# Optimization experiments

Measured on AMD Instinct MI355X. Metric: run time of the kernel, lower is better.

## Reference

```python
import jax, jax.numpy as jnp
import numpy as np

EMBED_DIM = 768
NUM_HEADS = 12
HEAD_DIM = EMBED_DIM // NUM_HEADS
B, T = 2, 2048


def setup_inputs() -> dict:
    key = jax.random.key(0)
    kx, kq, kqb, ko, kob = jax.random.split(key, 5)
    x = jax.random.normal(kx, (B, T, EMBED_DIM), dtype=jnp.float32)
    # xavier-uniform style params
    lim_qkv = float(np.sqrt(6.0 / (EMBED_DIM + 3 * EMBED_DIM)))
    qkv_kernel = jax.random.uniform(kq, (EMBED_DIM, 3 * EMBED_DIM), minval=-lim_qkv, maxval=lim_qkv, dtype=jnp.float32)
    qkv_bias = jnp.zeros((3 * EMBED_DIM,), dtype=jnp.float32)
    lim_o = float(np.sqrt(6.0 / (EMBED_DIM + EMBED_DIM)))
    o_kernel = jax.random.uniform(ko, (EMBED_DIM, EMBED_DIM), minval=-lim_o, maxval=lim_o, dtype=jnp.float32)
    o_bias = jnp.zeros((EMBED_DIM,), dtype=jnp.float32)
    return {"x": x, "qkv_kernel": qkv_kernel, "qkv_bias": qkv_bias, "o_kernel": o_kernel, "o_bias": o_bias}


def reference(x, qkv_kernel, qkv_bias, o_kernel, o_bias):
    b, t, d = x.shape
    # fused QKV projection
    qkv = jnp.einsum('btd,de->bte', x, qkv_kernel) + qkv_bias  # [B,T,3D]
    qkv = qkv.reshape(b, t, 3, NUM_HEADS, HEAD_DIM).transpose(2, 0, 3, 1, 4)  # [3,B,H,T,Dh]
    q, k, v = qkv[0], qkv[1], qkv[2]
    # naive attention: materializes full [B,H,T,T] scores (as in original)
    scale = 1.0 / np.sqrt(HEAD_DIM).astype(np.float32)
    attn_logits = jnp.einsum('bhqd,bhkd->bhqk', q, k) * scale
    attention = jax.nn.softmax(attn_logits, axis=-1)
    values = jnp.einsum('bhqk,bhkd->bhqd', attention, v)
    values = values.transpose(0, 2, 1, 3).reshape(b, t, d)  # [B,T,D]
    o = jnp.einsum('btd,de->bte', values, o_kernel) + o_bias
    return (o, attention)
```

## Files before the change

### kernel.cpp

```cpp
#include <hip/hip_runtime.h>
#include <hip/hip_bf16.h>
#include <hip/hip_fp16.h>

typedef _Float16 f16;
typedef _Float16 f16x4 __attribute__((ext_vector_type(4)));
typedef _Float16 f16x8 __attribute__((ext_vector_type(8)));
typedef float f32x4 __attribute__((ext_vector_type(4)));

#define MFMA16(a, b, c) __builtin_amdgcn_mfma_f32_16x16x32_f16(a, b, c, 0, 0, 0)

__device__ __forceinline__ float fexp2(float x) {
#if __has_builtin(__builtin_amdgcn_exp2f)
    return __builtin_amdgcn_exp2f(x);
#else
    return exp2f(x);
#endif
}

typedef __attribute__((address_space(1))) const void gconst_t;
typedef __attribute__((address_space(3))) void lds_t;
__device__ __forceinline__ void gload16(const f16* g, f16* l) {
    __builtin_amdgcn_global_load_lds((gconst_t*)g, (lds_t*)l, 16, 0, 0);
}

__global__ void k_convert_x(const float* __restrict__ in, f16* __restrict__ out, int n4) {
    int i = blockIdx.x * blockDim.x + threadIdx.x;
    if (i >= n4) return;
    float4 v = ((const float4*)in)[i];
    f16x4 o = {(f16)v.x, (f16)v.y, (f16)v.z, (f16)v.w};
    ((f16x4*)out)[i] = o;
}

__global__ __launch_bounds__(256) void k_transpose(const float* __restrict__ in,
                                                   f16* __restrict__ out, int K, int N) {
    __shared__ f16 tile[64][72];
    int n0 = blockIdx.x * 64, k0 = blockIdx.y * 64;
    int t = threadIdx.x;
    int r = t >> 2, cb = (t & 3) * 16;
    const float* src = in + (size_t)(k0 + r) * N + n0 + cb;
#pragma unroll
    for (int j = 0; j < 4; ++j) {
        float4 v = ((const float4*)src)[j];
        tile[r][cb + 4 * j + 0] = (f16)v.x;
        tile[r][cb + 4 * j + 1] = (f16)v.y;
        tile[r][cb + 4 * j + 2] = (f16)v.z;
        tile[r][cb + 4 * j + 3] = (f16)v.w;
    }
    __syncthreads();
    int nl = t >> 2, kb = (t & 3) * 16;
    f16* dst = out + (size_t)(n0 + nl) * K + k0 + kb;
#pragma unroll
    for (int j = 0; j < 2; ++j) {
        f16x8 o;
#pragma unroll
        for (int e = 0; e < 8; ++e) o[e] = tile[kb + 8 * j + e][nl];
        *(f16x8*)(dst + 8 * j) = o;
    }
}

__device__ __forceinline__ void gemm_core(const f16* __restrict__ A, const f16* __restrict__ Bt,
                                          int m0, int n0, int lane, int w, int wr, int wc,
                                          f16* As, f16* Bs, f32x4 acc[4][4]) {
    int prow = lane >> 2, pc = lane & 3;
    int lrow = prow ^ ((prow >> 2) & 1);
    int lcol = (pc ^ (lrow & 3)) * 8;
    int rsw = (lane & 7) << 3;
    for (int kt = 0; kt < 24; ++kt) {
        const f16* ab = A + (size_t)(m0 + w * 32 + lrow) * 768 + kt * 32 + lcol;
        const f16* bb = Bt + (size_t)(n0 + w * 32 + lrow) * 768 + kt * 32 + lcol;
        gload16(ab, As + (w * 32) * 32);
        gload16(ab + (size_t)16 * 768, As + (w * 32 + 16) * 32);
        gload16(bb, Bs + (w * 32) * 32);
        gload16(bb + (size_t)16 * 768, Bs + (w * 32 + 16) * 32);
        __syncthreads();
        f16x8 a[4], b[4];
#pragma unroll
        for (int i = 0; i < 4; ++i) {
            int idx = (wr * 64 + i * 16 + (lane & 15)) * 32 + (lane >> 4) * 8;
            a[i] = *(const f16x8*)(As + (idx ^ rsw));
        }
#pragma unroll
        for (int j = 0; j < 4; ++j) {
            int idx = (wc * 64 + j * 16 + (lane & 15)) * 32 + (lane >> 4) * 8;
            b[j] = *(const f16x8*)(Bs + (idx ^ rsw));
        }
#pragma unroll
        for (int i = 0; i < 4; ++i)
#pragma unroll
            for (int j = 0; j < 4; ++j) acc[i][j] = MFMA16(a[i], b[j], acc[i][j]);
        __syncthreads();
    }
}

__global__ __launch_bounds__(256) void k_qkv_gemm(const f16* __restrict__ A, const f16* __restrict__ Bt,
                                                  const float* __restrict__ bias,
                                                  f16* __restrict__ Qh, f16* __restrict__ Kf,
                                                  f16* __restrict__ Vf) {
    __shared__ __align__(16) f16 As[128 * 32];
    __shared__ __align__(16) f16 Bs[128 * 32];
    int m0 = blockIdx.x * 128, n0 = blockIdx.y * 128;
    int t = threadIdx.x, lane = t & 63, w = t >> 6;
    int wr = w >> 1, wc = w & 1;
    f32x4 zero = {0.f, 0.f, 0.f, 0.f};
    f32x4 acc[4][4];
#pragma unroll
    for (int i = 0; i < 4; ++i)
#pragma unroll
        for (int j = 0; j < 4; ++j) acc[i][j] = zero;

    gemm_core(A, Bt, m0, n0, lane, w, wr, wc, As, Bs, acc);

    const float QSCALE = 0.18033688011112042f;
#pragma unroll
    for (int j = 0; j < 4; ++j) {
        int n = n0 + wc * 64 + j * 16 + (lane & 15);
        int which = n / 768;
        int rem = n - which * 768;
        int h = rem >> 6, d = rem & 63;
        float bv = bias[n];
#pragma unroll
        for (int i = 0; i < 4; ++i) {
            int m = m0 + wr * 64 + i * 16 + ((lane >> 4) << 2);
            int bb = m >> 11, tt = m & 2047;
            int bh = bb * 12 + h;
            if (which == 2) {
                int kt = tt >> 6;
                int half = (tt & 63) >> 5, hi = (tt & 31) >> 3, e0 = tt & 7;
                int jd = d >> 4, lo = d & 15;
                size_t addr = (((size_t)bh * 32 + kt) * 8 + jd * 2 + half) * 512 +
                              (size_t)(hi * 16 + lo) * 8 + e0;
                f16x4 pk;
#pragma unroll
                for (int r = 0; r < 4; ++r) pk[r] = (f16)(acc[i][j][r] + bv);
                *(f16x4*)(Vf + addr) = pk;
            } else if (which == 0) {
#pragma unroll
                for (int r = 0; r < 4; ++r)
                    Qh[((size_t)bh * 2048 + tt + r) * 64 + d] = (f16)((acc[i][j][r] + bv) * QSCALE);
            } else {
                int half = d >> 5, hi = (d & 31) >> 3, e = d & 7;
#pragma unroll
                for (int r = 0; r < 4; ++r) {
                    int tr = tt + r;
                    int kt = tr >> 6, row = tr & 63;
                    int s = row >> 4, lo = row & 15;
                    size_t addr = (((size_t)bh * 32 + kt) * 8 + s * 2 + half) * 512 +
                                  (size_t)(hi * 16 + lo) * 8 + e;
                    Kf[addr] = (f16)(acc[i][j][r] + bv);
                }
            }
        }
    }
}

__global__ __launch_bounds__(256) void k_o_gemm(const f16* __restrict__ A, const f16* __restrict__ Bt,
                                                const float* __restrict__ bias,
                                                float* __restrict__ out) {
    __shared__ __align__(16) f16 As[128 * 32];
    __shared__ __align__(16) f16 Bs[128 * 32];
    int m0 = blockIdx.x * 128, n0 = blockIdx.y * 128;
    int t = threadIdx.x, lane = t & 63, w = t >> 6;
    int wr = w >> 1, wc = w & 1;
    f32x4 zero = {0.f, 0.f, 0.f, 0.f};
    f32x4 acc[4][4];
#pragma unroll
    for (int i = 0; i < 4; ++i)
#pragma unroll
        for (int j = 0; j < 4; ++j) acc[i][j] = zero;

    gemm_core(A, Bt, m0, n0, lane, w, wr, wc, As, Bs, acc);

#pragma unroll
    for (int j = 0; j < 4; ++j) {
        int n = n0 + wc * 64 + j * 16 + (lane & 15);
        float bv = bias[n];
#pragma unroll
        for (int i = 0; i < 4; ++i) {
            int m = m0 + wr * 64 + i * 16 + ((lane >> 4) << 2);
#pragma unroll
            for (int r = 0; r < 4; ++r) out[(size_t)(m + r) * 768 + n] = acc[i][j][r] + bv;
        }
    }
}

__global__ __launch_bounds__(256) void k_lsum(const f16* __restrict__ Qh, const f16* __restrict__ Kf,
                                              float* __restrict__ lpart) {
    int qt = blockIdx.x, bh = blockIdx.y, kc = blockIdx.z;
    int q0 = qt * 64;
    int t = threadIdx.x, lane = t & 63, w = t >> 6;
    const f16* qbase = Qh + ((size_t)bh * 2048 + q0 + w * 16) * 64;
    const f16* kfb = Kf + (size_t)bh * 32 * 4096 + (size_t)lane * 8;

    f16x8 aq[2];
#pragma unroll
    for (int f = 0; f < 2; ++f)
        aq[f] = *(const f16x8*)(qbase + (size_t)(lane & 15) * 64 + f * 32 + (lane >> 4) * 8);
    f32x4 zero = {0.f, 0.f, 0.f, 0.f};

    auto LOADK = [&](f16x8* dst, int kt) {
        const f16* kp = kfb + (size_t)kt * 4096;
#pragma unroll
        for (int f = 0; f < 8; ++f) dst[f] = *(const f16x8*)(kp + f * 512);
    };
    auto QKTS = [&](const f16x8* kf, f32x4* s4) {
#pragma unroll
        for (int s = 0; s < 4; ++s) {
            s4[s] = MFMA16(kf[2 * s], aq[0], zero);
            s4[s] = MFMA16(kf[2 * s + 1], aq[1], s4[s]);
        }
    };

    f16x8 ka[8], kb2[8];
    float lsum = 0.f;
    int base = kc * 8;
    LOADK(ka, base);
    for (int i = 0; i < 8; i += 2) {
        f32x4 s4[4];
        LOADK(kb2, base + i + 1);
        QKTS(ka, s4);
#pragma unroll
        for (int s = 0; s < 4; ++s)
#pragma unroll
            for (int r = 0; r < 4; ++r) lsum += fexp2(s4[s][r]);
        LOADK(ka, base + ((i + 2) & 7));
        QKTS(kb2, s4);
#pragma unroll
        for (int s = 0; s < 4; ++s)
#pragma unroll
            for (int r = 0; r < 4; ++r) lsum += fexp2(s4[s][r]);
    }
    lsum += __shfl_xor(lsum, 16, 64);
    lsum += __shfl_xor(lsum, 32, 64);
    float* lp = lpart + (size_t)kc * 49152 + (size_t)bh * 2048 + q0 + w * 16;
    if (lane < 16) lp[lane] = lsum;
}

__global__ __launch_bounds__(256, 3) void k_attn(const f16* __restrict__ Qh, const f16* __restrict__ Kf,
                                                 const f16* __restrict__ Vf,
                                                 const float* __restrict__ lpart,
                                                 float* __restrict__ attn, f16* __restrict__ valh) {
    __shared__ __align__(16) float Ps32_all[4][16 * 68];
    int orig = blockIdx.x;
    int swz = (orig & 7) * 96 + (orig >> 3);
    int bh = swz >> 5, qt = swz & 31;
    int q0 = qt * 64;
    int t = threadIdx.x, lane = t & 63, w = t >> 6;

    const f16* qbase = Qh + ((size_t)bh * 2048 + q0 + w * 16) * 64;
    const f16* kfb = Kf + (size_t)bh * 32 * 4096 + (size_t)lane * 8;
    const f16* vfb = Vf + (size_t)bh * 32 * 4096 + (size_t)lane * 8;

    f16x8 aq[2];
#pragma unroll
    for (int f = 0; f < 2; ++f)
        aq[f] = *(const f16x8*)(qbase + (size_t)(lane & 15) * 64 + f * 32 + (lane >> 4) * 8);
    f32x4 zero = {0.f, 0.f, 0.f, 0.f};

    float linv;
    {
        size_t qoff = (size_t)bh * 2048 + q0 + w * 16 + (lane & 15);
        float s = 0.f;
#pragma unroll
        for (int kc = 0; kc < 4; ++kc) s += lpart[(size_t)kc * 49152 + qoff];
        linv = 1.0f / s;
    }

    auto LOADK = [&](f16x8* dst, int kt) {
        const f16* kp = kfb + (size_t)kt * 4096;
#pragma unroll
        for (int f = 0; f < 8; ++f) dst[f] = *(const f16x8*)(kp + f * 512);
    };
    auto QKTS = [&](const f16x8* kf, f32x4* s4) {
#pragma unroll
        for (int s = 0; s < 4; ++s) {
            s4[s] = MFMA16(kf[2 * s], aq[0], zero);
            s4[s] = MFMA16(kf[2 * s + 1], aq[1], s4[s]);
        }
    };

    f32x4 accv[4];
#pragma unroll
    for (int j = 0; j < 4; ++j) accv[j] = zero;
    float* Ps = Ps32_all[w];
    float* attn_base = attn + ((size_t)bh * 2048 + q0 + w * 16) * 2048;
    f16x8 ka[8], kb2[8], vbuf[8];

    auto step2 = [&](f16x8* curK, f16x8* nxtK, int kt) {
        {
            const f16* vp = vfb + (size_t)kt * 4096;
#pragma unroll
            for (int f = 0; f < 8; ++f) vbuf[f] = *(const f16x8*)(vp + f * 512);
        }
        LOADK(nxtK, (kt + 1) & 31);
        f32x4 s4[4];
        QKTS(curK, s4);
#pragma unroll
        for (int s = 0; s < 4; ++s) {
            f32x4 pv;
#pragma unroll
            for (int r = 0; r < 4; ++r) pv[r] = fexp2(s4[s][r]) * linv;
            *(f32x4*)(Ps + (lane & 15) * 68 + s * 16 + (lane >> 4) * 4) = pv;
        }
        f16x8 pa[2];
#pragma unroll
        for (int half = 0; half < 2; ++half) {
            const float* pr = Ps + (lane & 15) * 68 + half * 32 + (lane >> 4) * 8;
            f32x4 lo = *(const f32x4*)(pr);
            f32x4 hi = *(const f32x4*)(pr + 4);
            f16x8 pf = {(f16)lo[0], (f16)lo[1], (f16)lo[2], (f16)lo[3],
                        (f16)hi[0], (f16)hi[1], (f16)hi[2], (f16)hi[3]};
            pa[half] = pf;
        }
        float* ab = attn_base + kt * 64;
#pragma unroll
        for (int i = 0; i < 4; ++i) {
            int row = i * 4 + (lane >> 4);
            int col = (lane & 15) * 4;
            f32x4 v = *(const f32x4*)(Ps + row * 68 + col);
            *(f32x4*)(ab + (size_t)row * 2048 + col) = v;
        }
#pragma unroll
        for (int jd = 0; jd < 4; ++jd) {
            accv[jd] = MFMA16(pa[0], vbuf[2 * jd], accv[jd]);
            accv[jd] = MFMA16(pa[1], vbuf[2 * jd + 1], accv[jd]);
        }
    };

    LOADK(ka, 0);
    for (int kt = 0; kt < 32; kt += 2) {
        step2(ka, kb2, kt);
        step2(kb2, ka, kt + 1);
    }

    int b = bh / 12, h = bh - b * 12;
#pragma unroll
    for (int j = 0; j < 4; ++j) {
#pragma unroll
        for (int r = 0; r < 4; ++r) {
            int rowg = b * 2048 + q0 + w * 16 + (lane >> 4) * 4 + r;
            int col = h * 64 + j * 16 + (lane & 15);
            valh[(size_t)rowg * 768 + col] = (f16)accv[j][r];
        }
    }
}

extern "C" void kernel_launch(void* const* d_in, const int* in_sizes, int n_in,
                              void* d_out, int out_size, void* d_ws, size_t ws_size,
                              hipStream_t stream) {
    const float* x = (const float*)d_in[0];
    const float* wqkv = (const float*)d_in[1];
    const float* bqkv = (const float*)d_in[2];
    const float* wo = (const float*)d_in[3];
    const float* bo = (const float*)d_in[4];

    float* out_o = (float*)d_out;
    float* out_attn = out_o + (size_t)2 * 2048 * 768;

    f16* ws = (f16*)d_ws;
    f16* xh = ws;
    f16* wqkv_t = xh + 3145728;
    f16* wo_t = wqkv_t + 1769472;
    f16* Qh = wo_t + 589824;
    f16* Kf = Qh + 3145728;
    f16* Vf = Kf + 3145728;
    f16* valh = Vf + 3145728;
    float* lpart = (float*)(valh + 3145728);

    k_convert_x<<<3072, 256, 0, stream>>>(x, xh, 786432);
    k_transpose<<<dim3(36, 12), 256, 0, stream>>>(wqkv, wqkv_t, 768, 2304);
    k_transpose<<<dim3(12, 12), 256, 0, stream>>>(wo, wo_t, 768, 768);
    k_qkv_gemm<<<dim3(32, 18), 256, 0, stream>>>(xh, wqkv_t, bqkv, Qh, Kf, Vf);
    k_lsum<<<dim3(32, 24, 4), 256, 0, stream>>>(Qh, Kf, lpart);
    k_attn<<<768, 256, 0, stream>>>(Qh, Kf, Vf, lpart, out_attn, valh);
    k_o_gemm<<<dim3(32, 6), 256, 0, stream>>>(valh, wo_t, bo, out_o);
}
```

Measured before the change: 203.2 us.

## Stage K/V tiles through LDS in attention, merge prep kernels, add MFMA priority

The attention kernel now loads each K/V tile once per block into double-buffered LDS with global_load_lds, instead of every wave loading the full tiles into registers. This is meant to cut redundant global traffic and register pressure, at the cost of a block-wide barrier every iteration and more LDS per block, which may lower occupancy. The three preprocessing launches (x conversion and two weight transposes) are merged into one kernel to save launch overhead. s_setprio hints are placed around the MFMA sections in the lsum and attention kernels.

```diff
diff --git a/kernel.cpp b/kernel.cpp
--- a/kernel.cpp
+++ b/kernel.cpp
@@ -23,19 +23,9 @@
     __builtin_amdgcn_global_load_lds((gconst_t*)g, (lds_t*)l, 16, 0, 0);
 }
 
-__global__ void k_convert_x(const float* __restrict__ in, f16* __restrict__ out, int n4) {
-    int i = blockIdx.x * blockDim.x + threadIdx.x;
-    if (i >= n4) return;
-    float4 v = ((const float4*)in)[i];
-    f16x4 o = {(f16)v.x, (f16)v.y, (f16)v.z, (f16)v.w};
-    ((f16x4*)out)[i] = o;
-}
-
-__global__ __launch_bounds__(256) void k_transpose(const float* __restrict__ in,
-                                                   f16* __restrict__ out, int K, int N) {
-    __shared__ f16 tile[64][72];
-    int n0 = blockIdx.x * 64, k0 = blockIdx.y * 64;
-    int t = threadIdx.x;
+__device__ __forceinline__ void transpose_body(const float* __restrict__ in, f16* __restrict__ out,
+                                               int K, int N, int n0, int k0, int t,
+                                               f16 (*tile)[72]) {
     int r = t >> 2, cb = (t & 3) * 16;
     const float* src = in + (size_t)(k0 + r) * N + n0 + cb;
 #pragma unroll
@@ -55,6 +45,27 @@
 #pragma unroll
         for (int e = 0; e < 8; ++e) o[e] = tile[kb + 8 * j + e][nl];
         *(f16x8*)(dst + 8 * j) = o;
+    }
+}
+
+__global__ __launch_bounds__(256) void k_prep(const float* __restrict__ x,
+                                              const float* __restrict__ wqkv,
+                                              const float* __restrict__ wo,
+                                              f16* __restrict__ xh, f16* __restrict__ wqkv_t,
+                                              f16* __restrict__ wo_t) {
+    __shared__ f16 tile[64][72];
+    int bid = blockIdx.x, t = threadIdx.x;
+    if (bid < 3072) {
+        int i = bid * 256 + t;
+        float4 v = ((const float4*)x)[i];
+        f16x4 o = {(f16)v.x, (f16)v.y, (f16)v.z, (f16)v.w};
+        ((f16x4*)xh)[i] = o;
+    } else if (bid < 3504) {
+        int idx = bid - 3072;
+        transpose_body(wqkv, wqkv_t, 768, 2304, (idx % 36) * 64, (idx / 36) * 64, t, tile);
+    } else {
+        int idx = bid - 3504;
+        transpose_body(wo, wo_t, 768, 768, (idx % 12) * 64, (idx / 12) * 64, t, tile);
     }
 }
 
@@ -203,11 +214,13 @@
         for (int f = 0; f < 8; ++f) dst[f] = *(const f16x8*)(kp + f * 512);
     };
     auto QKTS = [&](const f16x8* kf, f32x4* s4) {
+        __builtin_amdgcn_s_setprio(1);
 #pragma unroll
         for (int s = 0; s < 4; ++s) {
             s4[s] = MFMA16(kf[2 * s], aq[0], zero);
             s4[s] = MFMA16(kf[2 * s + 1], aq[1], s4[s]);
         }
+        __builtin_amdgcn_s_setprio(0);
     };
 
     f16x8 ka[8], kb2[8];
@@ -239,6 +252,7 @@
                                                  const f16* __restrict__ Vf,
                                                  const float* __restrict__ lpart,
                                                  float* __restrict__ attn, f16* __restrict__ valh) {
+    __shared__ __align__(16) f16 KV[2][8192];
     __shared__ __align__(16) float Ps32_all[4][16 * 68];
     int orig = blockIdx.x;
     int swz = (orig & 7) * 96 + (orig >> 3);
@@ -247,8 +261,8 @@
     int t = threadIdx.x, lane = t & 63, w = t >> 6;
 
     const f16* qbase = Qh + ((size_t)bh * 2048 + q0 + w * 16) * 64;
-    const f16* kfb = Kf + (size_t)bh * 32 * 4096 + (size_t)lane * 8;
-    const f16* vfb = Vf + (size_t)bh * 32 * 4096 + (size_t)lane * 8;
+    const f16* kfT = Kf + (size_t)bh * 32 * 4096;
+    const f16* vfT = Vf + (size_t)bh * 32 * 4096;
 
     f16x8 aq[2];
 #pragma unroll
@@ -265,17 +279,15 @@
         linv = 1.0f / s;
     }
 
-    auto LOADK = [&](f16x8* dst, int kt) {
-        const f16* kp = kfb + (size_t)kt * 4096;
-#pragma unroll
-        for (int f = 0; f < 8; ++f) dst[f] = *(const f16x8*)(kp + f * 512);
-    };
-    auto QKTS = [&](const f16x8* kf, f32x4* s4) {
-#pragma unroll
-        for (int s = 0; s < 4; ++s) {
-            s4[s] = MFMA16(kf[2 * s], aq[0], zero);
-            s4[s] = MFMA16(kf[2 * s + 1], aq[1], s4[s]);
-        }
+    auto STAGE = [&](int buf, int kt) {
+        const f16* kp = kfT + (size_t)kt * 4096 + (size_t)lane * 8;
+        const f16* vp = vfT + (size_t)kt * 4096 + (size_t)lane * 8;
+        f16* kb = &KV[buf][0];
+        f16* vb = &KV[buf][4096];
+        gload16(kp + (2 * w) * 512, kb + (2 * w) * 512);
+        gload16(kp + (2 * w + 1) * 512, kb + (2 * w + 1) * 512);
+        gload16(vp + (2 * w) * 512, vb + (2 * w) * 512);
+        gload16(vp + (2 * w + 1) * 512, vb + (2 * w + 1) * 512);
     };
 
     f32x4 accv[4];
@@ -283,17 +295,24 @@
     for (int j = 0; j < 4; ++j) accv[j] = zero;
     float* Ps = Ps32_all[w];
     float* attn_base = attn + ((size_t)bh * 2048 + q0 + w * 16) * 2048;
-    f16x8 ka[8], kb2[8], vbuf[8];
-
-    auto step2 = [&](f16x8* curK, f16x8* nxtK, int kt) {
-        {
-            const f16* vp = vfb + (size_t)kt * 4096;
-#pragma unroll
-            for (int f = 0; f < 8; ++f) vbuf[f] = *(const f16x8*)(vp + f * 512);
-        }
-        LOADK(nxtK, (kt + 1) & 31);
+
+    STAGE(0, 0);
+    __syncthreads();
+    int cur = 0;
+    for (int kt = 0; kt < 32; ++kt) {
+        if (kt < 31) STAGE(cur ^ 1, kt + 1);
+        const f16* Ks = &KV[cur][0];
+        const f16* Vs = &KV[cur][4096];
         f32x4 s4[4];
-        QKTS(curK, s4);
+        __builtin_amdgcn_s_setprio(1);
+#pragma unroll
+        for (int s = 0; s < 4; ++s) {
+            f16x8 k0 = *(const f16x8*)(Ks + (2 * s) * 512 + lane * 8);
+            f16x8 k1 = *(const f16x8*)(Ks + (2 * s + 1) * 512 + lane * 8);
+            s4[s] = MFMA16(k0, aq[0], zero);
+            s4[s] = MFMA16(k1, aq[1], s4[s]);
+        }
+        __builtin_amdgcn_s_setprio(0);
 #pragma unroll
         for (int s = 0; s < 4; ++s) {
             f32x4 pv;
@@ -303,13 +322,13 @@
         }
         f16x8 pa[2];
 #pragma unroll
-        for (int half = 0; half < 2; ++half) {
-            const float* pr = Ps + (lane & 15) * 68 + half * 32 + (lane >> 4) * 8;
+        for (int hh = 0; hh < 2; ++hh) {
+            const float* pr = Ps + (lane & 15) * 68 + hh * 32 + (lane >> 4) * 8;
             f32x4 lo = *(const f32x4*)(pr);
             f32x4 hi = *(const f32x4*)(pr + 4);
             f16x8 pf = {(f16)lo[0], (f16)lo[1], (f16)lo[2], (f16)lo[3],
                         (f16)hi[0], (f16)hi[1], (f16)hi[2], (f16)hi[3]};
-            pa[half] = pf;
+            pa[hh] = pf;
         }
         float* ab = attn_base + kt * 64;
 #pragma unroll
@@ -319,17 +338,17 @@
             f32x4 v = *(const f32x4*)(Ps + row * 68 + col);
             *(f32x4*)(ab + (size_t)row * 2048 + col) = v;
         }
+        __builtin_amdgcn_s_setprio(1);
 #pragma unroll
         for (int jd = 0; jd < 4; ++jd) {
-            accv[jd] = MFMA16(pa[0], vbuf[2 * jd], accv[jd]);
-            accv[jd] = MFMA16(pa[1], vbuf[2 * jd + 1], accv[jd]);
-        }
-    };
-
-    LOADK(ka, 0);
-    for (int kt = 0; kt < 32; kt += 2) {
-        step2(ka, kb2, kt);
-        step2(kb2, ka, kt + 1);
+            f16x8 v0 = *(const f16x8*)(Vs + (2 * jd) * 512 + lane * 8);
+            f16x8 v1 = *(const f16x8*)(Vs + (2 * jd + 1) * 512 + lane * 8);
+            accv[jd] = MFMA16(pa[0], v0, accv[jd]);
+            accv[jd] = MFMA16(pa[1], v1, accv[jd]);
+        }
+        __builtin_amdgcn_s_setprio(0);
+        __syncthreads();
+        cur ^= 1;
     }
 
     int b = bh / 12, h = bh - b * 12;
@@ -366,9 +385,7 @@
     f16* valh = Vf + 3145728;
     float* lpart = (float*)(valh + 3145728);
 
-    k_convert_x<<<3072, 256, 0, stream>>>(x, xh, 786432);
-    k_transpose<<<dim3(36, 12), 256, 0, stream>>>(wqkv, wqkv_t, 768, 2304);
-    k_transpose<<<dim3(12, 12), 256, 0, stream>>>(wo, wo_t, 768, 768);
+    k_prep<<<3648, 256, 0, stream>>>(x, wqkv, wo, xh, wqkv_t, wo_t);
     k_qkv_gemm<<<dim3(32, 18), 256, 0, stream>>>(xh, wqkv_t, bqkv, Qh, Kf, Vf);
     k_lsum<<<dim3(32, 24, 4), 256, 0, stream>>>(Qh, Kf, lpart);
     k_attn<<<768, 256, 0, stream>>>(Qh, Kf, Vf, lpart, out_attn, valh);
```

Measured after the change: 188.4 us. 7.3% less time.
